# Kernel tuning notes

Hardware: AMD Instinct MI355X
Metric: run time of the kernel (lower is better)

## Reference

```python
import jax, jax.numpy as jnp
import numpy as np

NUM_EMBEDDINGS = 1024
EMBEDDING_DIM = 256
COMMITMENT_COST = 0.25


def setup_inputs() -> dict:
    key = jax.random.key(0)
    k1, k2 = jax.random.split(key)
    inputs = jax.random.normal(k1, (32, EMBEDDING_DIM, 32, 32), dtype=jnp.float32)
    # nn.Embedding weight init: uniform(-1/K, 1/K)
    embeddings = (jax.random.uniform(k2, (NUM_EMBEDDINGS, EMBEDDING_DIM), dtype=jnp.float32) * 2.0 - 1.0) / NUM_EMBEDDINGS
    return {"inputs": inputs, "embeddings": embeddings}


def reference(inputs, embeddings):
    B, D, H, W = inputs.shape
    K = embeddings.shape[0]
    # [B,D,H,W] -> [N,D] with N = B*H*W
    flat = jnp.transpose(inputs, (0, 2, 3, 1)).reshape(-1, D)
    distances = (jnp.sum(flat * flat, axis=1, keepdims=True)
                 + jnp.sum(embeddings * embeddings, axis=1)
                 - 2.0 * jnp.matmul(flat, embeddings.T))
    encoding_indices = jnp.argmin(distances, axis=1)  # [N]
    # gather codebook vectors (same math as one-hot @ embeddings)
    quantized = embeddings[encoding_indices]  # [N,D]
    quantized = quantized.reshape(B, H, W, D).transpose(0, 3, 1, 2)  # [B,D,H,W]
    e_latent_loss = jnp.mean((jax.lax.stop_gradient(quantized) - inputs) ** 2)
    q_latent_loss = jnp.mean((quantized - jax.lax.stop_gradient(inputs)) ** 2)
    loss = q_latent_loss + COMMITMENT_COST * e_latent_loss
    # straight-through estimator
    quantized_st = inputs + jax.lax.stop_gradient(quantized - inputs)
    # perplexity from one-hot average (counts / N)
    counts = jnp.zeros((K,), dtype=flat.dtype).at[encoding_indices].add(1.0)
    avg_probs = counts / flat.shape[0]
    perplexity = jnp.exp(-jnp.sum(avg_probs * jnp.log(avg_probs + 1e-10)))
    return quantized_st, loss, perplexity, encoding_indices.reshape(B, H, W)
```

## Files before the change

### kernel.cpp

```cpp
#include <hip/hip_runtime.h>


#define NROWS 32768
#define CAPA 16384
#define CAPB 8192
#define GAP_TAU 1e-4f

typedef __attribute__((ext_vector_type(8))) short short8;
typedef __attribute__((ext_vector_type(8))) unsigned short ushort8;
typedef __attribute__((ext_vector_type(4))) float f32x4;

struct Top4 { float v0, v1, v2, v3; int i0, i1, i2; };

__device__ __forceinline__ void top4_init(Top4& t) {
    t.v0 = t.v1 = t.v2 = t.v3 = 3.4e38f;
    t.i0 = t.i1 = t.i2 = 0x7fffffff;
}
__device__ __forceinline__ void top4_insert(Top4& t, float cv, int ci) {
    if (cv < t.v3) {
        if (cv < t.v2) {
            t.v3 = t.v2;
            if (cv < t.v1) {
                t.v2 = t.v1; t.i2 = t.i1;
                if (cv < t.v0) { t.v1 = t.v0; t.i1 = t.i0; t.v0 = cv; t.i0 = ci; }
                else           { t.v1 = cv; t.i1 = ci; }
            } else { t.v2 = cv; t.i2 = ci; }
        } else { t.v3 = cv; }
    }
}
__device__ __forceinline__ void top4_merge(Top4& t, const Top4& o) {
    top4_insert(t, o.v0, o.i0);
    top4_insert(t, o.v1, o.i1);
    top4_insert(t, o.v2, o.i2);
    t.v3 = fminf(t.v3, o.v3);
}

__device__ __forceinline__ unsigned short bf16_rne(float v) {
    unsigned int u = __float_as_uint(v);
    return (unsigned short)((u + 0x7fffu + ((u >> 16) & 1u)) >> 16);
}
__device__ __forceinline__ float bf16_to_f(unsigned short h) {
    return __uint_as_float(((unsigned int)h) << 16);
}

__device__ __forceinline__ void gl16(const void* g, void* l) {
    __builtin_amdgcn_global_load_lds(
        (const __attribute__((address_space(1))) unsigned int*)g,
        (__attribute__((address_space(3))) unsigned int*)l, 16, 0, 0);
}

template <int STRIDE>
__device__ __forceinline__ float np_sumsq256(const float* __restrict__ p) {
    float half[2];
#pragma unroll
    for (int h = 0; h < 2; ++h) {
        float r[8];
#pragma unroll
        for (int j = 0; j < 8; ++j) {
            const float v = p[(size_t)(h * 128 + j) * STRIDE];
            r[j] = __fmul_rn(v, v);
        }
        for (int i = 8; i < 128; i += 8) {
#pragma unroll
            for (int j = 0; j < 8; ++j) {
                const float v = p[(size_t)(h * 128 + i + j) * STRIDE];
                r[j] = __fadd_rn(r[j], __fmul_rn(v, v));
            }
        }
        half[h] = __fadd_rn(__fadd_rn(__fadd_rn(r[0], r[1]), __fadd_rn(r[2], r[3])),
                            __fadd_rn(__fadd_rn(r[4], r[5]), __fadd_rn(r[6], r[7])));
    }
    return __fadd_rn(half[0], half[1]);
}

__global__ void prep_kernel(const float* __restrict__ emb, const float* __restrict__ x,
                            float* __restrict__ ee, float* __restrict__ xx,
                            unsigned short* __restrict__ EhT, unsigned short* __restrict__ ElT,
                            unsigned short* __restrict__ XhT, unsigned short* __restrict__ XlT) {
    if (blockIdx.x < 4) {
        const int k = blockIdx.x * 256 + threadIdx.x;
        ee[k] = np_sumsq256<1>(emb + (size_t)k * 256);
        return;
    }
    if (blockIdx.x >= 260) {
        const int n = (blockIdx.x - 260) * 256 + threadIdx.x;
        const int b = n >> 10, p = n & 1023;
        const float* xb = x + (size_t)b * 262144 + p;
        float r[8];
        float half0 = 0.f, half1 = 0.f;
        for (int dc = 0; dc < 8; ++dc) {
            float v[32];
#pragma unroll
            for (int j = 0; j < 32; ++j)
                v[j] = xb[(size_t)(dc * 32 + j) * 1024];
            if ((dc & 3) == 0) {
#pragma unroll
                for (int j = 0; j < 8; ++j) r[j] = __fmul_rn(v[j], v[j]);
#pragma unroll
                for (int g = 1; g < 4; ++g)
#pragma unroll
                    for (int j = 0; j < 8; ++j)
                        r[j] = __fadd_rn(r[j], __fmul_rn(v[g * 8 + j], v[g * 8 + j]));
            } else {
#pragma unroll
                for (int g = 0; g < 4; ++g)
#pragma unroll
                    for (int j = 0; j < 8; ++j)
                        r[j] = __fadd_rn(r[j], __fmul_rn(v[g * 8 + j], v[g * 8 + j]));
            }
            if ((dc & 3) == 3) {
                const float s = __fadd_rn(
                    __fadd_rn(__fadd_rn(r[0], r[1]), __fadd_rn(r[2], r[3])),
                    __fadd_rn(__fadd_rn(r[4], r[5]), __fadd_rn(r[6], r[7])));
                if (dc == 3) half0 = s; else half1 = s;
            }
            const size_t xrow = ((size_t)dc * NROWS + n) * 32;
#pragma unroll
            for (int g = 0; g < 4; ++g) {
                ushort8 H, L;
#pragma unroll
                for (int j = 0; j < 8; ++j) {
                    const float vv = v[g * 8 + j];
                    const unsigned int u = __float_as_uint(vv);
                    H[j] = (unsigned short)(u >> 16);
                    const float rr = vv - __uint_as_float(u & 0xFFFF0000u);
                    L[j] = (unsigned short)(__float_as_uint(rr) >> 16);
                }
                *(ushort8*)(XhT + xrow + g * 8) = H;
                *(ushort8*)(XlT + xrow + g * 8) = L;
            }
        }
        xx[n] = __fadd_rn(half0, half1);
        return;
    }
    const int eid = (blockIdx.x - 4) * 256 + threadIdx.x;
    const int code = eid >> 6;
    const int d0 = (eid & 63) * 4;
    float4 v = *(const float4*)(emb + (size_t)code * 256 + d0);
    const float vv[4] = {v.x, v.y, v.z, v.w};
    unsigned short h[4], l[4];
#pragma unroll
    for (int i = 0; i < 4; ++i) {
        h[i] = bf16_rne(vv[i]);
        l[i] = bf16_rne(vv[i] - bf16_to_f(h[i]));
    }
    const size_t o = ((size_t)(d0 >> 5) * 1024 + code) * 32 + (d0 & 31);
    *(ushort4*)(EhT + o) = make_ushort4(h[0], h[1], h[2], h[3]);
    *(ushort4*)(ElT + o) = make_ushort4(l[0], l[1], l[2], l[3]);
}

__global__ __launch_bounds__(256, 4)
void mfma_argmin_kernel(const unsigned short* __restrict__ XhT, const unsigned short* __restrict__ XlT,
                        const unsigned short* __restrict__ EhT, const unsigned short* __restrict__ ElT,
                        const float* __restrict__ ee, const float* __restrict__ xx,
                        float* __restrict__ pv0, float* __restrict__ pv1,
                        float* __restrict__ pv2, float* __restrict__ pv3,
                        int* __restrict__ pi0, int* __restrict__ pi1, int* __restrict__ pi2) {
    __shared__ __attribute__((aligned(16))) unsigned short Eh_s[128 * 32];
    __shared__ __attribute__((aligned(16))) unsigned short El_s[128 * 32];
    __shared__ __attribute__((aligned(16))) unsigned short Xh_s[128 * 32];
    __shared__ __attribute__((aligned(16))) unsigned short Xl_s[128 * 32];
    __shared__ float eeLds[128];
    __shared__ float mV0[128], mV1[128], mV2[128], mV3[128];
    __shared__ int   mI0[128], mI1[128], mI2[128];

    const int t = threadIdx.x;
    const int w = t >> 6, lane = t & 63;
    const int lane15 = lane & 15, quad = lane >> 4;
    const int nblk = blockIdx.x & 255, cblk = blockIdx.x >> 8;
    const int n0 = nblk * 128, c0 = cblk * 128;

    if (t < 128) eeLds[t] = ee[c0 + t];

    f32x4 acc[4][4];
#pragma unroll
    for (int i = 0; i < 4; ++i)
#pragma unroll
        for (int j = 0; j < 4; ++j) acc[i][j] = (f32x4){0.f, 0.f, 0.f, 0.f};

    for (int dc = 0; dc < 8; ++dc) {
        if (dc) __syncthreads();
        const size_t xoff = ((size_t)dc * NROWS + n0) * 32;
        const size_t eoff = ((size_t)dc * 1024 + c0) * 32;
#pragma unroll
        for (int k = 0; k < 2; ++k) {
            const int id = k * 256 + t;
            const int ldso = (k * 256 + w * 64) * 8;
            gl16(XhT + xoff + (size_t)id * 8, &Xh_s[ldso]);
            gl16(XlT + xoff + (size_t)id * 8, &Xl_s[ldso]);
            gl16(EhT + eoff + (size_t)id * 8, &Eh_s[ldso]);
            gl16(ElT + eoff + (size_t)id * 8, &El_s[ldso]);
        }
        __syncthreads();
        short8 ah[4], al[4], bhf[4], blf[4];
#pragma unroll
        for (int i = 0; i < 4; ++i) {
            const int cr = (w >> 1) * 64 + i * 16 + lane15;
            ah[i] = *(const short8*)&Eh_s[cr * 32 + quad * 8];
            al[i] = *(const short8*)&El_s[cr * 32 + quad * 8];
        }
#pragma unroll
        for (int j = 0; j < 4; ++j) {
            const int nr = (w & 1) * 64 + j * 16 + lane15;
            bhf[j] = *(const short8*)&Xh_s[nr * 32 + quad * 8];
            blf[j] = *(const short8*)&Xl_s[nr * 32 + quad * 8];
        }
#pragma unroll
        for (int i = 0; i < 4; ++i)
#pragma unroll
            for (int j = 0; j < 4; ++j) {
                acc[i][j] = __builtin_amdgcn_mfma_f32_16x16x32_bf16(al[i], bhf[j], acc[i][j], 0, 0, 0);
                acc[i][j] = __builtin_amdgcn_mfma_f32_16x16x32_bf16(ah[i], blf[j], acc[i][j], 0, 0, 0);
                acc[i][j] = __builtin_amdgcn_mfma_f32_16x16x32_bf16(ah[i], bhf[j], acc[i][j], 0, 0, 0);
            }
    }
    Top4 tj[4];
#pragma unroll
    for (int j = 0; j < 4; ++j) {
        const float xxv = xx[n0 + (w & 1) * 64 + j * 16 + lane15];
        Top4 tt; top4_init(tt);
#pragma unroll
        for (int i = 0; i < 4; ++i)
#pragma unroll
            for (int r = 0; r < 4; ++r) {
                const int cl = (w >> 1) * 64 + i * 16 + quad * 4 + r;
                const float t1 = __fadd_rn(xxv, eeLds[cl]);
                const float s = __fmaf_rn(-2.0f, acc[i][j][r], t1);
                top4_insert(tt, s, c0 + cl);
            }
#pragma unroll
        for (int off = 16; off <= 32; off <<= 1) {
            Top4 o;
            o.v0 = __shfl_xor(tt.v0, off, 64); o.i0 = __shfl_xor(tt.i0, off, 64);
            o.v1 = __shfl_xor(tt.v1, off, 64); o.i1 = __shfl_xor(tt.i1, off, 64);
            o.v2 = __shfl_xor(tt.v2, off, 64); o.i2 = __shfl_xor(tt.i2, off, 64);
            o.v3 = __shfl_xor(tt.v3, off, 64);
            top4_merge(tt, o);
        }
        tj[j] = tt;
    }
    __syncthreads();
    if (w >= 2 && quad == 0) {
#pragma unroll
        for (int j = 0; j < 4; ++j) {
            const int idx = (w & 1) * 64 + j * 16 + lane15;
            mV0[idx] = tj[j].v0; mV1[idx] = tj[j].v1; mV2[idx] = tj[j].v2; mV3[idx] = tj[j].v3;
            mI0[idx] = tj[j].i0; mI1[idx] = tj[j].i1; mI2[idx] = tj[j].i2;
        }
    }
    __syncthreads();
    if (w < 2 && quad == 0) {
#pragma unroll
        for (int j = 0; j < 4; ++j) {
            const int idx = w * 64 + j * 16 + lane15;
            Top4 tt = tj[j];
            Top4 o;
            o.v0 = mV0[idx]; o.v1 = mV1[idx]; o.v2 = mV2[idx]; o.v3 = mV3[idx];
            o.i0 = mI0[idx]; o.i1 = mI1[idx]; o.i2 = mI2[idx];
            top4_merge(tt, o);
            const size_t g = (size_t)cblk * NROWS + n0 + idx;
            pv0[g] = tt.v0; pv1[g] = tt.v1; pv2[g] = tt.v2; pv3[g] = tt.v3;
            pi0[g] = tt.i0; pi1[g] = tt.i1; pi2[g] = tt.i2;
        }
    }
}

__global__ void combine_kernel(const float* __restrict__ pv0, const float* __restrict__ pv1,
                               const float* __restrict__ pv2, const float* __restrict__ pv3,
                               const int* __restrict__ pi0, const int* __restrict__ pi1,
                               const int* __restrict__ pi2,
                               int* __restrict__ fidx, float* __restrict__ outIdx,
                               int* __restrict__ counts,
                               int* __restrict__ listA, int* __restrict__ nA,
                               int* __restrict__ listB, int* __restrict__ nB) {
    const int n = blockIdx.x * blockDim.x + threadIdx.x;
    if (n >= NROWS) return;
    float v0[8], v1[8], v2[8]; int i0[8], i1[8], i2[8];
    float b1 = 3.4e38f, v4m = 3.4e38f;
#pragma unroll
    for (int s = 0; s < 8; ++s) {
        const size_t g = (size_t)s * NROWS + n;
        v0[s] = pv0[g]; v1[s] = pv1[g]; v2[s] = pv2[g];
        i0[s] = pi0[g]; i1[s] = pi1[g]; i2[s] = pi2[g];
        b1 = fminf(b1, v0[s]);
        v4m = fminf(v4m, pv3[g]);
    }
    if (v4m - b1 < GAP_TAU) {
        const int s = atomicAdd(nB, 1);
        if (s < CAPB) { listB[s] = n; return; }
    } else {
        int ks[24]; int cnt = 0;
#pragma unroll
        for (int s = 0; s < 8; ++s) {
            if (v0[s] - b1 < GAP_TAU) ks[cnt++] = i0[s];
            if (v1[s] - b1 < GAP_TAU) ks[cnt++] = i1[s];
            if (v2[s] - b1 < GAP_TAU) ks[cnt++] = i2[s];
        }
        if (cnt > 1) {
            const int slot = atomicAdd(nA, 1);
            if (slot < CAPA) {
                int* e = listA + (size_t)slot * 32;
                e[0] = n; e[1] = cnt;
                for (int c = 0; c < cnt; ++c) e[2 + c] = ks[c];
                return;
            }
            const int s2 = atomicAdd(nB, 1);
            if (s2 < CAPB) { listB[s2] = n; return; }
        }
        const int bi = ks[0];
        fidx[n] = bi;
        outIdx[n] = (float)bi;
        atomicAdd(&counts[bi], 1);
        return;
    }
    int bi = 0x7fffffff;
#pragma unroll
    for (int s = 0; s < 8; ++s) if (v0[s] == b1 && i0[s] < bi) bi = i0[s];
    fidx[n] = bi; outIdx[n] = (float)bi; atomicAdd(&counts[bi], 1);
}

__global__ __launch_bounds__(256)
void exact_kernel(const float* __restrict__ x, const float* __restrict__ emb,
                  const float* __restrict__ ee, const float* __restrict__ xx,
                  const int* __restrict__ listA, const int* __restrict__ nA,
                  int* __restrict__ fidx, float* __restrict__ outIdx,
                  int* __restrict__ counts) {
    int total = *nA; if (total > CAPA) total = CAPA;
    const int sub = threadIdx.x >> 5;
    const int li  = threadIdx.x & 31;
    for (int e = blockIdx.x * 8 + sub; e < total; e += gridDim.x * 8) {
        const int* ent = listA + (size_t)e * 32;
        const int n = ent[0], cnt = ent[1];
        float s = 3.4e38f; int k = 0x7fffffff;
        if (li < cnt) {
            k = ent[2 + li];
            const int b = n >> 10, p = n & 1023;
            const float* xr = x + (size_t)b * 262144 + p;
            const float* er = emb + (size_t)k * 256;
            float dot = 0.f;
#pragma unroll 8
            for (int d = 0; d < 256; ++d)
                dot = __fmaf_rn(er[d], xr[(size_t)d * 1024], dot);
            s = __fmaf_rn(-2.0f, dot, __fadd_rn(xx[n], ee[k]));
        }
#pragma unroll
        for (int off = 1; off < 32; off <<= 1) {
            const float ov = __shfl_xor(s, off, 32);
            const int   ok = __shfl_xor(k, off, 32);
            if (ov < s || (ov == s && ok < k)) { s = ov; k = ok; }
        }
        if (li == 0) { fidx[n] = k; outIdx[n] = (float)k; atomicAdd(&counts[k], 1); }
    }
}

__global__ __launch_bounds__(256)
void rescanB_kernel(const float* __restrict__ x, const float* __restrict__ emb,
                    const float* __restrict__ ee, const float* __restrict__ xx,
                    const int* __restrict__ listB, const int* __restrict__ nB,
                    int* __restrict__ fidx, float* __restrict__ outIdx,
                    int* __restrict__ counts) {
    __shared__ float xrow[256];
    __shared__ float bV[4];
    __shared__ int   bI[4];
    int total = *nB; if (total > CAPB) total = CAPB;
    for (int wq = blockIdx.x; wq < total; wq += gridDim.x) {
        const int n = listB[wq];
        const int b = n >> 10, p = n & 1023;
        const float* xb = x + (size_t)b * 262144 + p;
        xrow[threadIdx.x] = xb[(size_t)threadIdx.x * 1024];
        __syncthreads();
        const float xxn = xx[n];
        float best = 3.4e38f; int bi = 0x7fffffff;
        for (int k = threadIdx.x; k < 1024; k += 256) {
            const float* e = emb + (size_t)k * 256;
            float dot = 0.f;
            for (int d = 0; d < 256; ++d) dot = __fmaf_rn(e[d], xrow[d], dot);
            const float t1 = __fadd_rn(xxn, ee[k]);
            const float s = __fmaf_rn(-2.0f, dot, t1);
            if (s < best) { best = s; bi = k; }
        }
        for (int off = 32; off > 0; off >>= 1) {
            const float ov = __shfl_down(best, off, 64);
            const int   oi = __shfl_down(bi,   off, 64);
            if (ov < best || (ov == best && oi < bi)) { best = ov; bi = oi; }
        }
        const int lane = threadIdx.x & 63, wv = threadIdx.x >> 6;
        if (lane == 0) { bV[wv] = best; bI[wv] = bi; }
        __syncthreads();
        if (threadIdx.x == 0) {
            float bb = bV[0]; int ii = bI[0];
            for (int i = 1; i < 4; ++i)
                if (bV[i] < bb || (bV[i] == bb && bI[i] < ii)) { bb = bV[i]; ii = bI[i]; }
            fidx[n] = ii;
            outIdx[n] = (float)ii;
            atomicAdd(&counts[ii], 1);
        }
        __syncthreads();
    }
}

__global__ __launch_bounds__(256)
void quantize_kernel(const float* __restrict__ x, const float* __restrict__ emb,
                     const int* __restrict__ fidx, float* __restrict__ out,
                     float* __restrict__ sumsq) {
    const int tid = blockIdx.x * 256 + threadIdx.x;
    const int dchunk = tid >> 15;
    const int n = tid & 32767;
    const int b = n >> 10, p = n & 1023;
    const int d0 = dchunk * 64;
    const int k = fidx[n];
    const float4* er = (const float4*)(emb + (size_t)k * 256 + d0);
    const float* xr = x + (size_t)b * 262144 + (size_t)d0 * 1024 + p;
    float* orow = out + (size_t)b * 262144 + (size_t)d0 * 1024 + p;
    float loc = 0.f;
#pragma unroll
    for (int j = 0; j < 16; ++j) {
        const float4 qv = er[j];
        const float q[4] = {qv.x, qv.y, qv.z, qv.w};
#pragma unroll
        for (int i = 0; i < 4; ++i) {
            const size_t off = (size_t)(j * 4 + i) * 1024;
            const float xv = xr[off];
            const float e = q[i] - xv;
            orow[off] = xv + e;
            loc = fmaf(e, e, loc);
        }
    }
    for (int off = 32; off > 0; off >>= 1) loc += __shfl_down(loc, off, 64);
    __shared__ float red[4];
    const int lane = threadIdx.x & 63, wv = threadIdx.x >> 6;
    if (lane == 0) red[wv] = loc;
    __syncthreads();
    if (threadIdx.x == 0) atomicAdd(sumsq, red[0] + red[1] + red[2] + red[3]);
}

__global__ void finalize_kernel(const int* __restrict__ counts, const float* __restrict__ sumsq,
                                float* __restrict__ outScalars) {
    const int k = threadIdx.x;
    const float p = (float)counts[k] * (1.0f / 32768.0f);
    float term = p * logf(p + 1e-10f);
    for (int off = 32; off > 0; off >>= 1) term += __shfl_down(term, off, 64);
    __shared__ float red[16];
    const int lane = k & 63, wv = k >> 6;
    if (lane == 0) red[wv] = term;
    __syncthreads();
    if (k == 0) {
        float s = 0.f;
        for (int i = 0; i < 16; ++i) s += red[i];
        const float m = sumsq[0] * (1.0f / 8388608.0f);
        outScalars[0] = 1.25f * m;
        outScalars[1] = expf(-s);
    }
}

extern "C" void kernel_launch(void* const* d_in, const int* in_sizes, int n_in,
                              void* d_out, int out_size, void* d_ws, size_t ws_size,
                              hipStream_t stream) {
    const float* x   = (const float*)d_in[0];
    const float* emb = (const float*)d_in[1];
    float* out = (float*)d_out;
    float* W   = (float*)d_ws;
    float* sumsq = W;
    int*   nA    = (int*)(W + 1);
    int*   nB    = (int*)(W + 2);
    int*   counts = (int*)(W + 64);
    float* ee    = W + 1088;
    float* xx    = W + 2112;
    float* pv0   = W + 34880;
    float* pv1   = W + 297024;
    float* pv2   = W + 559168;
    float* pv3   = W + 821312;
    int*   pi0   = (int*)(W + 1083456);
    int*   pi1   = (int*)(W + 1345600);
    int*   pi2   = (int*)(W + 1607744);
    int*   listA = (int*)(W + 1869888);
    int*   listB = (int*)(W + 2394176);
    unsigned short* EhT = (unsigned short*)(W + 2402368);
    unsigned short* ElT = (unsigned short*)(W + 2533440);
    int*   fidx  = (int*)(W + 2664512);
    unsigned short* XhT = (unsigned short*)(W + 2697280);
    unsigned short* XlT = (unsigned short*)(W + 6891584);

    hipMemsetAsync(W, 0, 1088 * sizeof(float), stream);
    prep_kernel<<<388, 256, 0, stream>>>(emb, x, ee, xx, EhT, ElT, XhT, XlT);
    mfma_argmin_kernel<<<2048, 256, 0, stream>>>(XhT, XlT, EhT, ElT, ee, xx,
                                                 pv0, pv1, pv2, pv3, pi0, pi1, pi2);
    combine_kernel<<<128, 256, 0, stream>>>(pv0, pv1, pv2, pv3, pi0, pi1, pi2,
                                            fidx, out + 8388610, counts, listA, nA, listB, nB);
    exact_kernel<<<512, 256, 0, stream>>>(x, emb, ee, xx, listA, nA, fidx, out + 8388610, counts);
    rescanB_kernel<<<64, 256, 0, stream>>>(x, emb, ee, xx, listB, nB, fidx, out + 8388610, counts);
    quantize_kernel<<<512, 256, 0, stream>>>(x, emb, fidx, out, sumsq);
    finalize_kernel<<<1, 1024, 0, stream>>>(counts, sumsq, out + 8388608);
}
```

Measured before the change: 219.2 us.

## Double-buffer MFMA tiles, swizzle LDS layout, and merge small kernels

The MFMA argmin kernel now double-buffers its shared-memory tiles, prefetching the next D-chunk while the current one is computed, and uses XOR-swizzled row slots in both the prep-written layouts and the LDS reads to avoid bank conflicts. Occupancy bounds drop to 2 blocks per CU to make room for the doubled LDS. The final partial top-4 write is staged through LDS for coalesced stores. The memset is folded into an extra prep block, and the exact and rescan kernels are merged into one launch, which cuts launch overhead but makes those stages share a grid.

```diff
diff --git a/kernel.cpp b/kernel.cpp
--- a/kernel.cpp
+++ b/kernel.cpp
@@ -76,7 +76,12 @@
 __global__ void prep_kernel(const float* __restrict__ emb, const float* __restrict__ x,
                             float* __restrict__ ee, float* __restrict__ xx,
                             unsigned short* __restrict__ EhT, unsigned short* __restrict__ ElT,
-                            unsigned short* __restrict__ XhT, unsigned short* __restrict__ XlT) {
+                            unsigned short* __restrict__ XhT, unsigned short* __restrict__ XlT,
+                            float* __restrict__ wzero) {
+    if (blockIdx.x >= 388) {
+        for (int i = threadIdx.x; i < 1088; i += 256) wzero[i] = 0.f;
+        return;
+    }
     if (blockIdx.x < 4) {
         const int k = blockIdx.x * 256 + threadIdx.x;
         ee[k] = np_sumsq256<1>(emb + (size_t)k * 256);
@@ -86,6 +91,7 @@
         const int n = (blockIdx.x - 260) * 256 + threadIdx.x;
         const int b = n >> 10, p = n & 1023;
         const float* xb = x + (size_t)b * 262144 + p;
+        const int kk = (n >> 1) & 3;
         float r[8];
         float half0 = 0.f, half1 = 0.f;
         for (int dc = 0; dc < 8; ++dc) {
@@ -126,8 +132,8 @@
                     const float rr = vv - __uint_as_float(u & 0xFFFF0000u);
                     L[j] = (unsigned short)(__float_as_uint(rr) >> 16);
                 }
-                *(ushort8*)(XhT + xrow + g * 8) = H;
-                *(ushort8*)(XlT + xrow + g * 8) = L;
+                *(ushort8*)(XhT + xrow + (g ^ kk) * 8) = H;
+                *(ushort8*)(XlT + xrow + (g ^ kk) * 8) = L;
             }
         }
         xx[n] = __fadd_rn(half0, half1);
@@ -144,22 +150,26 @@
         h[i] = bf16_rne(vv[i]);
         l[i] = bf16_rne(vv[i] - bf16_to_f(h[i]));
     }
-    const size_t o = ((size_t)(d0 >> 5) * 1024 + code) * 32 + (d0 & 31);
+    const int kk = (code >> 1) & 3;
+    const int slot = (d0 & 31) >> 3;
+    const int within = (d0 & 31) & 7;
+    const size_t o = ((size_t)(d0 >> 5) * 1024 + code) * 32
+                   + (size_t)((slot ^ kk) * 8 + within);
     *(ushort4*)(EhT + o) = make_ushort4(h[0], h[1], h[2], h[3]);
     *(ushort4*)(ElT + o) = make_ushort4(l[0], l[1], l[2], l[3]);
 }
 
-__global__ __launch_bounds__(256, 4)
+__global__ __launch_bounds__(256, 2)
 void mfma_argmin_kernel(const unsigned short* __restrict__ XhT, const unsigned short* __restrict__ XlT,
                         const unsigned short* __restrict__ EhT, const unsigned short* __restrict__ ElT,
                         const float* __restrict__ ee, const float* __restrict__ xx,
                         float* __restrict__ pv0, float* __restrict__ pv1,
                         float* __restrict__ pv2, float* __restrict__ pv3,
                         int* __restrict__ pi0, int* __restrict__ pi1, int* __restrict__ pi2) {
-    __shared__ __attribute__((aligned(16))) unsigned short Eh_s[128 * 32];
-    __shared__ __attribute__((aligned(16))) unsigned short El_s[128 * 32];
-    __shared__ __attribute__((aligned(16))) unsigned short Xh_s[128 * 32];
-    __shared__ __attribute__((aligned(16))) unsigned short Xl_s[128 * 32];
+    __shared__ __attribute__((aligned(16))) unsigned short Eh_s[2][4096];
+    __shared__ __attribute__((aligned(16))) unsigned short El_s[2][4096];
+    __shared__ __attribute__((aligned(16))) unsigned short Xh_s[2][4096];
+    __shared__ __attribute__((aligned(16))) unsigned short Xl_s[2][4096];
     __shared__ float eeLds[128];
     __shared__ float mV0[128], mV1[128], mV2[128], mV3[128];
     __shared__ int   mI0[128], mI1[128], mI2[128];
@@ -172,48 +182,68 @@
 
     if (t < 128) eeLds[t] = ee[c0 + t];
 
+    const int fslot = (quad ^ ((lane15 >> 1) & 3)) * 8;
+    int eoffs[4], xoffs[4];
+#pragma unroll
+    for (int i = 0; i < 4; ++i)
+        eoffs[i] = ((w >> 1) * 64 + i * 16 + lane15) * 32 + fslot;
+#pragma unroll
+    for (int j = 0; j < 4; ++j)
+        xoffs[j] = ((w & 1) * 64 + j * 16 + lane15) * 32 + fslot;
+
     f32x4 acc[4][4];
 #pragma unroll
     for (int i = 0; i < 4; ++i)
 #pragma unroll
         for (int j = 0; j < 4; ++j) acc[i][j] = (f32x4){0.f, 0.f, 0.f, 0.f};
 
-    for (int dc = 0; dc < 8; ++dc) {
-        if (dc) __syncthreads();
+    auto STAGE = [&](int dc, int bb) {
         const size_t xoff = ((size_t)dc * NROWS + n0) * 32;
         const size_t eoff = ((size_t)dc * 1024 + c0) * 32;
 #pragma unroll
         for (int k = 0; k < 2; ++k) {
             const int id = k * 256 + t;
             const int ldso = (k * 256 + w * 64) * 8;
-            gl16(XhT + xoff + (size_t)id * 8, &Xh_s[ldso]);
-            gl16(XlT + xoff + (size_t)id * 8, &Xl_s[ldso]);
-            gl16(EhT + eoff + (size_t)id * 8, &Eh_s[ldso]);
-            gl16(ElT + eoff + (size_t)id * 8, &El_s[ldso]);
-        }
-        __syncthreads();
-        short8 ah[4], al[4], bhf[4], blf[4];
+            gl16(XhT + xoff + (size_t)id * 8, &Xh_s[bb][ldso]);
+            gl16(XlT + xoff + (size_t)id * 8, &Xl_s[bb][ldso]);
+            gl16(EhT + eoff + (size_t)id * 8, &Eh_s[bb][ldso]);
+            gl16(ElT + eoff + (size_t)id * 8, &El_s[bb][ldso]);
+        }
+    };
+
+    STAGE(0, 0);
+    asm volatile("s_waitcnt vmcnt(0)" ::: "memory");
+    __builtin_amdgcn_s_barrier();
+    asm volatile("" ::: "memory");
+
+#pragma unroll 2
+    for (int dc = 0; dc < 8; ++dc) {
+        const int bb = dc & 1;
+        if (dc < 7) STAGE(dc + 1, bb ^ 1);
+        short8 ah[4], al[4], bh[4], bl[4];
 #pragma unroll
         for (int i = 0; i < 4; ++i) {
-            const int cr = (w >> 1) * 64 + i * 16 + lane15;
-            ah[i] = *(const short8*)&Eh_s[cr * 32 + quad * 8];
-            al[i] = *(const short8*)&El_s[cr * 32 + quad * 8];
+            ah[i] = *(const short8*)&Eh_s[bb][eoffs[i]];
+            al[i] = *(const short8*)&El_s[bb][eoffs[i]];
         }
 #pragma unroll
         for (int j = 0; j < 4; ++j) {
-            const int nr = (w & 1) * 64 + j * 16 + lane15;
-            bhf[j] = *(const short8*)&Xh_s[nr * 32 + quad * 8];
-            blf[j] = *(const short8*)&Xl_s[nr * 32 + quad * 8];
+            bh[j] = *(const short8*)&Xh_s[bb][xoffs[j]];
+            bl[j] = *(const short8*)&Xl_s[bb][xoffs[j]];
         }
 #pragma unroll
         for (int i = 0; i < 4; ++i)
 #pragma unroll
             for (int j = 0; j < 4; ++j) {
-                acc[i][j] = __builtin_amdgcn_mfma_f32_16x16x32_bf16(al[i], bhf[j], acc[i][j], 0, 0, 0);
-                acc[i][j] = __builtin_amdgcn_mfma_f32_16x16x32_bf16(ah[i], blf[j], acc[i][j], 0, 0, 0);
-                acc[i][j] = __builtin_amdgcn_mfma_f32_16x16x32_bf16(ah[i], bhf[j], acc[i][j], 0, 0, 0);
-            }
-    }
+                acc[i][j] = __builtin_amdgcn_mfma_f32_16x16x32_bf16(al[i], bh[j], acc[i][j], 0, 0, 0);
+                acc[i][j] = __builtin_amdgcn_mfma_f32_16x16x32_bf16(ah[i], bl[j], acc[i][j], 0, 0, 0);
+                acc[i][j] = __builtin_amdgcn_mfma_f32_16x16x32_bf16(ah[i], bh[j], acc[i][j], 0, 0, 0);
+            }
+        asm volatile("s_waitcnt vmcnt(0)" ::: "memory");
+        __builtin_amdgcn_s_barrier();
+        asm volatile("" ::: "memory");
+    }
+
     Top4 tj[4];
 #pragma unroll
     for (int j = 0; j < 4; ++j) {
@@ -239,7 +269,6 @@
         }
         tj[j] = tt;
     }
-    __syncthreads();
     if (w >= 2 && quad == 0) {
 #pragma unroll
         for (int j = 0; j < 4; ++j) {
@@ -258,10 +287,15 @@
             o.v0 = mV0[idx]; o.v1 = mV1[idx]; o.v2 = mV2[idx]; o.v3 = mV3[idx];
             o.i0 = mI0[idx]; o.i1 = mI1[idx]; o.i2 = mI2[idx];
             top4_merge(tt, o);
-            const size_t g = (size_t)cblk * NROWS + n0 + idx;
-            pv0[g] = tt.v0; pv1[g] = tt.v1; pv2[g] = tt.v2; pv3[g] = tt.v3;
-            pi0[g] = tt.i0; pi1[g] = tt.i1; pi2[g] = tt.i2;
-        }
+            mV0[idx] = tt.v0; mV1[idx] = tt.v1; mV2[idx] = tt.v2; mV3[idx] = tt.v3;
+            mI0[idx] = tt.i0; mI1[idx] = tt.i1; mI2[idx] = tt.i2;
+        }
+    }
+    __syncthreads();
+    if (t < 128) {
+        const size_t g = (size_t)cblk * NROWS + n0 + t;
+        pv0[g] = mV0[t]; pv1[g] = mV1[t]; pv2[g] = mV2[t]; pv3[g] = mV3[t];
+        pi0[g] = mI0[t]; pi1[g] = mI1[t]; pi2[g] = mI2[t];
     }
 }
 
@@ -320,50 +354,46 @@
 }
 
 __global__ __launch_bounds__(256)
-void exact_kernel(const float* __restrict__ x, const float* __restrict__ emb,
-                  const float* __restrict__ ee, const float* __restrict__ xx,
-                  const int* __restrict__ listA, const int* __restrict__ nA,
-                  int* __restrict__ fidx, float* __restrict__ outIdx,
-                  int* __restrict__ counts) {
-    int total = *nA; if (total > CAPA) total = CAPA;
-    const int sub = threadIdx.x >> 5;
-    const int li  = threadIdx.x & 31;
-    for (int e = blockIdx.x * 8 + sub; e < total; e += gridDim.x * 8) {
-        const int* ent = listA + (size_t)e * 32;
-        const int n = ent[0], cnt = ent[1];
-        float s = 3.4e38f; int k = 0x7fffffff;
-        if (li < cnt) {
-            k = ent[2 + li];
-            const int b = n >> 10, p = n & 1023;
-            const float* xr = x + (size_t)b * 262144 + p;
-            const float* er = emb + (size_t)k * 256;
-            float dot = 0.f;
-#pragma unroll 8
-            for (int d = 0; d < 256; ++d)
-                dot = __fmaf_rn(er[d], xr[(size_t)d * 1024], dot);
-            s = __fmaf_rn(-2.0f, dot, __fadd_rn(xx[n], ee[k]));
-        }
-#pragma unroll
-        for (int off = 1; off < 32; off <<= 1) {
-            const float ov = __shfl_xor(s, off, 32);
-            const int   ok = __shfl_xor(k, off, 32);
-            if (ov < s || (ov == s && ok < k)) { s = ov; k = ok; }
-        }
-        if (li == 0) { fidx[n] = k; outIdx[n] = (float)k; atomicAdd(&counts[k], 1); }
-    }
-}
-
-__global__ __launch_bounds__(256)
-void rescanB_kernel(const float* __restrict__ x, const float* __restrict__ emb,
+void resolve_kernel(const float* __restrict__ x, const float* __restrict__ emb,
                     const float* __restrict__ ee, const float* __restrict__ xx,
+                    const int* __restrict__ listA, const int* __restrict__ nA,
                     const int* __restrict__ listB, const int* __restrict__ nB,
                     int* __restrict__ fidx, float* __restrict__ outIdx,
                     int* __restrict__ counts) {
     __shared__ float xrow[256];
     __shared__ float bV[4];
     __shared__ int   bI[4];
+    if (blockIdx.x < 512) {
+        int total = *nA; if (total > CAPA) total = CAPA;
+        const int sub = threadIdx.x >> 5;
+        const int li  = threadIdx.x & 31;
+        for (int e = blockIdx.x * 8 + sub; e < total; e += 512 * 8) {
+            const int* ent = listA + (size_t)e * 32;
+            const int n = ent[0], cnt = ent[1];
+            float s = 3.4e38f; int k = 0x7fffffff;
+            if (li < cnt) {
+                k = ent[2 + li];
+                const int b = n >> 10, p = n & 1023;
+                const float* xr = x + (size_t)b * 262144 + p;
+                const float* er = emb + (size_t)k * 256;
+                float dot = 0.f;
+#pragma unroll 8
+                for (int d = 0; d < 256; ++d)
+                    dot = __fmaf_rn(er[d], xr[(size_t)d * 1024], dot);
+                s = __fmaf_rn(-2.0f, dot, __fadd_rn(xx[n], ee[k]));
+            }
+#pragma unroll
+            for (int off = 1; off < 32; off <<= 1) {
+                const float ov = __shfl_xor(s, off, 32);
+                const int   ok = __shfl_xor(k, off, 32);
+                if (ov < s || (ov == s && ok < k)) { s = ov; k = ok; }
+            }
+            if (li == 0) { fidx[n] = k; outIdx[n] = (float)k; atomicAdd(&counts[k], 1); }
+        }
+        return;
+    }
     int total = *nB; if (total > CAPB) total = CAPB;
-    for (int wq = blockIdx.x; wq < total; wq += gridDim.x) {
+    for (int wq = (int)blockIdx.x - 512; wq < total; wq += 64) {
         const int n = listB[wq];
         const int b = n >> 10, p = n & 1023;
         const float* xb = x + (size_t)b * 262144 + p;
@@ -481,14 +511,13 @@
     unsigned short* XhT = (unsigned short*)(W + 2697280);
     unsigned short* XlT = (unsigned short*)(W + 6891584);
 
-    hipMemsetAsync(W, 0, 1088 * sizeof(float), stream);
-    prep_kernel<<<388, 256, 0, stream>>>(emb, x, ee, xx, EhT, ElT, XhT, XlT);
+    prep_kernel<<<389, 256, 0, stream>>>(emb, x, ee, xx, EhT, ElT, XhT, XlT, W);
     mfma_argmin_kernel<<<2048, 256, 0, stream>>>(XhT, XlT, EhT, ElT, ee, xx,
                                                  pv0, pv1, pv2, pv3, pi0, pi1, pi2);
     combine_kernel<<<128, 256, 0, stream>>>(pv0, pv1, pv2, pv3, pi0, pi1, pi2,
                                             fidx, out + 8388610, counts, listA, nA, listB, nB);
-    exact_kernel<<<512, 256, 0, stream>>>(x, emb, ee, xx, listA, nA, fidx, out + 8388610, counts);
-    rescanB_kernel<<<64, 256, 0, stream>>>(x, emb, ee, xx, listB, nB, fidx, out + 8388610, counts);
+    resolve_kernel<<<576, 256, 0, stream>>>(x, emb, ee, xx, listA, nA, listB, nB,
+                                            fidx, out + 8388610, counts);
     quantize_kernel<<<512, 256, 0, stream>>>(x, emb, fidx, out, sumsq);
     finalize_kernel<<<1, 1024, 0, stream>>>(counts, sumsq, out + 8388608);
 }
```

After: 234.2 us. 6.8% more time.
